# Kernel tuning notes

Hardware: AMD Instinct MI355X
Metric: run time of the kernel (lower is better)

Reference implementation:

```python
import jax, jax.numpy as jnp
import numpy as np

INF = 1.0e6
SIGMA = 1.0
RADIUS = 2.5
M, N, H, K, C_IN, C_OUT = 50000, 50000, 32, 15, 128, 128
EXTENT = 10.0  # spatial extent of the random point cloud


def setup_inputs() -> dict:
    key = jax.random.key(0)
    k1, k2, k3, k4, k5, k6 = jax.random.split(key, 6)
    q_pts = jax.random.uniform(k1, (M, 3), dtype=jnp.float32) * EXTENT
    s_pts = jax.random.uniform(k2, (N, 3), dtype=jnp.float32) * EXTENT
    s_feats = jax.random.normal(k3, (N, C_IN), dtype=jnp.float32)
    neighb_inds = jax.random.randint(k4, (M, H), 0, N, dtype=jnp.int64)
    # kernel points: random points inside sphere of given radius (stand-in for load_kernels)
    kp = jax.random.normal(k5, (K, 3), dtype=jnp.float32)
    kp = kp / jnp.linalg.norm(kp, axis=1, keepdims=True) * (RADIUS * 0.66)
    kernel_points = kp.at[0].set(0.0)  # fixed center point
    # kaiming-uniform-like init
    bound = 1.0 / np.sqrt(C_IN)
    weights = jax.random.uniform(k6, (K, C_IN, C_OUT), dtype=jnp.float32,
                                 minval=-bound, maxval=bound)
    return {"q_pts": q_pts, "s_pts": s_pts, "s_feats": s_feats,
            "neighb_inds": neighb_inds, "kernel_points": kernel_points,
            "weights": weights}


def reference(q_pts, s_pts, s_feats, neighb_inds, kernel_points, weights):
    # pad support points with a far-away point so out-of-range indices get zero influence
    s_pts_pad = jnp.concatenate([s_pts, jnp.full((1, 3), INF, s_pts.dtype)], axis=0)
    neighbors = s_pts_pad[neighb_inds] - q_pts[:, None, :]          # (M, H, 3)
    diffs = neighbors[:, :, None, :] - kernel_points[None, None]    # (M, H, K, 3)
    sq_dist = jnp.sum(diffs * diffs, axis=-1)                       # (M, H, K)
    # linear influence, clipped at 0 (no_grad in torch -> stop_gradient here)
    w = jnp.clip(1.0 - jnp.sqrt(sq_dist) / SIGMA, 0.0)              # (M, H, K)
    neighbor_weights = jax.lax.stop_gradient(jnp.swapaxes(w, 1, 2)) # (M, K, H)
    # gather neighbor features (padded with a zero row)
    feats_pad = jnp.concatenate([s_feats, jnp.zeros((1, s_feats.shape[1]), s_feats.dtype)], axis=0)
    neighbor_feats = feats_pad[neighb_inds]                         # (M, H, C_in)
    weighted_feats = jnp.matmul(neighbor_weights, neighbor_feats)   # (M, K, C_in)
    return jnp.einsum('mkc,kcd->md', weighted_feats, weights)       # (M, C_out)
```

## Files before the change

### kernel.cpp

```cpp
#include <hip/hip_runtime.h>

#define M_Q 50000
#define N_S 50000
#define H_N 32
#define K_P 15
#define C_IN 128
#define C_OUT 128

#define G_QB 64
#define G_NT 256
#define NB_GEO ((M_Q + G_QB - 1) / G_QB)
#define LCAP 64
#define ACC_STRIDE 132

#define WTF_SLOTS (K_P * 8 * 4 * 64)
#define NB_WCVT (WTF_SLOTS / 256)
#define WS_NEED (WTF_SLOTS * 16)

typedef __attribute__((ext_vector_type(8))) short s8v;
typedef __attribute__((ext_vector_type(4))) float f4v;
typedef __attribute__((ext_vector_type(4))) float fl4;
typedef __attribute__((ext_vector_type(4))) unsigned u4v;

static __device__ __forceinline__ unsigned f2bf_bits(float x) {
    union { float f; unsigned u; } v; v.f = x;
    return (v.u + 0x7fffu + ((v.u >> 16) & 1u)) >> 16;
}
static __device__ __forceinline__ unsigned pack_bf16(float a, float b) {
    return f2bf_bits(a) | (f2bf_bits(b) << 16);
}

static __device__ __forceinline__ void lds_fadd(float* p, float v) {
    unsigned off = (unsigned)(unsigned long long)p;
    asm volatile("ds_add_f32 %0, %1" :: "v"(off), "v"(v));
}

__global__ __launch_bounds__(256) void k0_wcvt(
    const float* __restrict__ W, unsigned short* __restrict__ wtf)
{
    const int i = blockIdx.x * 256 + threadIdx.x;
    if (i >= WTF_SLOTS) return;
    const int lane = i & 63;
    const int kk = (i >> 6) & 3;
    const int col = (i >> 8) & 7;
    const int k = i >> 11;
    const int d = col * 16 + (lane & 15);
    const int c0 = kk * 32 + (lane >> 4) * 8;
    u4v g;
    unsigned short* gs = (unsigned short*)&g;
    #pragma unroll
    for (int j = 0; j < 8; ++j)
        gs[j] = (unsigned short)f2bf_bits(W[((size_t)k * 128 + c0 + j) * 128 + d]);
    *(u4v*)(wtf + (size_t)i * 8) = g;
}

template <typename IT>
__global__ __launch_bounds__(G_NT, 3) void kpconv_fused(
    const float* __restrict__ q_pts,
    const float* __restrict__ s_pts,
    const float* __restrict__ s_feats,
    const IT* __restrict__ inds,
    const float* __restrict__ kp,
    const unsigned short* __restrict__ wtf,
    float* __restrict__ out)
{
    __shared__ float s_kp[K_P * 3];
    __shared__ float s_q[G_QB * 3];
    __shared__ int s_lcnt[K_P];
    __shared__ uint2 s_le[K_P][LCAP];
    __shared__ float s_acc[G_QB][ACC_STRIDE];

    const int b = blockIdx.x;
    const int t = threadIdx.x;
    const int qbase = b * G_QB;

    if (t < K_P * 3) s_kp[t] = kp[t];
    if (t < K_P) s_lcnt[t] = 0;
    if (t < G_QB * 3) {
        const int g = qbase * 3 + t;
        s_q[t] = (g < M_Q * 3) ? q_pts[g] : 0.0f;
    }
    {
        fl4* a4 = (fl4*)&s_acc[0][0];
        const fl4 z = {0.0f, 0.0f, 0.0f, 0.0f};
        #pragma unroll
        for (int i = t; i < G_QB * ACC_STRIDE / 4; i += G_NT) a4[i] = z;
    }
    __syncthreads();

    #pragma unroll
    for (int it = 0; it < 8; ++it) {
        const int task = it * G_NT + t;
        const int q = task >> 5, h = task & 31;
        const int qg = qbase + q;
        if (qg < M_Q) {
            long long idx = (long long)inds[(size_t)qg * H_N + h];
            if ((unsigned long long)idx < (unsigned long long)N_S) {
                const int i32 = (int)idx;
                const float rx = s_pts[i32 * 3 + 0] - s_q[q * 3 + 0];
                const float ry = s_pts[i32 * 3 + 1] - s_q[q * 3 + 1];
                const float rz = s_pts[i32 * 3 + 2] - s_q[q * 3 + 2];
                #pragma unroll
                for (int k = 0; k < K_P; ++k) {
                    const float dx = rx - s_kp[k * 3 + 0];
                    const float dy = ry - s_kp[k * 3 + 1];
                    const float dz = rz - s_kp[k * 3 + 2];
                    const float d2 = dx * dx + dy * dy + dz * dz;
                    if (d2 < 1.0f) {
                        const float wgt = 1.0f - sqrtf(d2);
                        const int pos = atomicAdd(&s_lcnt[k], 1);
                        if (pos < LCAP)
                            s_le[k][pos] = make_uint2(((unsigned)q << 16) | (unsigned)i32,
                                                      __float_as_uint(wgt));
                    }
                }
            }
        }
    }
    __syncthreads();

    const int lane = t & 63;
    const int w = t >> 6;
    const int quad = lane >> 4, l15 = lane & 15;

    for (int k = w; k < K_P; k += 4) {
        const int cnt = min(s_lcnt[k], LCAP);
        const unsigned short* wk = wtf + (size_t)k * 2048 * 8;
        for (int sub = 0; sub * 16 < cnt; ++sub) {
            const int e = sub * 16 + l15;
            uint2 ent = make_uint2(0u, 0u);
            if (e < cnt) ent = s_le[k][e];
            const float wgt = __uint_as_float(ent.y);
            const float* fr = s_feats + (size_t)(ent.x & 0xffffu) * C_IN + quad * 8;
            s8v af[4];
            #pragma unroll
            for (int kk = 0; kk < 4; ++kk) {
                const fl4 a  = *(const fl4*)(fr + kk * 32);
                const fl4 bb = *(const fl4*)(fr + kk * 32 + 4);
                u4v g;
                g[0] = pack_bf16(wgt * a.x,  wgt * a.y);
                g[1] = pack_bf16(wgt * a.z,  wgt * a.w);
                g[2] = pack_bf16(wgt * bb.x, wgt * bb.y);
                g[3] = pack_bf16(wgt * bb.z, wgt * bb.w);
                af[kk] = *(s8v*)&g;
            }
            int m4[4];
            #pragma unroll
            for (int r = 0; r < 4; ++r) {
                const int er = sub * 16 + quad * 4 + r;
                m4[r] = (er < cnt) ? (int)(s_le[k][er].x >> 16) : -1;
            }
            #pragma unroll
            for (int nc = 0; nc < 8; ++nc) {
                s8v bfr[4];
                #pragma unroll
                for (int kk = 0; kk < 4; ++kk)
                    bfr[kk] = *(const s8v*)(wk + (size_t)((nc * 4 + kk) * 64 + lane) * 8);
                f4v acc = {0.0f, 0.0f, 0.0f, 0.0f};
                #pragma unroll
                for (int kk = 0; kk < 4; ++kk)
                    acc = __builtin_amdgcn_mfma_f32_16x16x32_bf16(af[kk], bfr[kk], acc, 0, 0, 0);
                #pragma unroll
                for (int r = 0; r < 4; ++r)
                    if (m4[r] >= 0)
                        lds_fadd(&s_acc[m4[r]][nc * 16 + l15], acc[r]);
            }
        }
    }
    asm volatile("s_waitcnt lgkmcnt(0)" ::: "memory");
    __syncthreads();

    const int mmax = min(G_QB, M_Q - qbase);
    #pragma unroll
    for (int it = 0; it < 8; ++it) {
        const int idx = it * G_NT + t;
        const int row = idx >> 5, c4 = (idx & 31) * 4;
        if (row < mmax)
            *(fl4*)(out + (size_t)(qbase + row) * C_OUT + c4) = *(const fl4*)&s_acc[row][c4];
    }
}

template <typename IT>
__global__ __launch_bounds__(128, 8) void kpconv_v1(
    const float* __restrict__ q_pts, const float* __restrict__ s_pts,
    const float* __restrict__ s_feats, const IT* __restrict__ neighb_inds,
    const float* __restrict__ kernel_points, const float* __restrict__ weights,
    float* __restrict__ out)
{
    __shared__ float s_kp[K_P * 3];
    __shared__ float s_w[K_P][H_N];
    __shared__ int s_idx[H_N];
    __shared__ unsigned s_hmask, s_kmask;
    __shared__ float s_wf[K_P][C_IN];
    const int m = blockIdx.x, tid = threadIdx.x;
    if (tid < K_P * 3) s_kp[tid] = kernel_points[tid];
    if (tid == 0) { s_hmask = 0u; s_kmask = 0u; }
    __syncthreads();
    if (tid < H_N) {
        long long idx = (long long)neighb_inds[(size_t)m * H_N + tid];
        const float qx = q_pts[m * 3], qy = q_pts[m * 3 + 1], qz = q_pts[m * 3 + 2];
        float rx, ry, rz; int idx32;
        if ((unsigned long long)idx < (unsigned long long)N_S) {
            idx32 = (int)idx;
            rx = s_pts[idx32 * 3] - qx; ry = s_pts[idx32 * 3 + 1] - qy; rz = s_pts[idx32 * 3 + 2] - qz;
        } else { idx32 = 0; rx = ry = rz = 1.0e6f; }
        s_idx[tid] = idx32;
        unsigned kmask = 0u;
        #pragma unroll
        for (int k = 0; k < K_P; ++k) {
            const float dx = rx - s_kp[k * 3], dy = ry - s_kp[k * 3 + 1], dz = rz - s_kp[k * 3 + 2];
            const float w = fmaxf(1.0f - sqrtf(dx * dx + dy * dy + dz * dz), 0.0f);
            s_w[k][tid] = w;
            if (w > 0.0f) kmask |= (1u << k);
        }
        if (kmask) { atomicOr(&s_hmask, 1u << tid); atomicOr(&s_kmask, kmask); }
    }
    __syncthreads();
    const unsigned hmask = s_hmask, kmask = s_kmask;
    float wf[K_P];
    #pragma unroll
    for (int k = 0; k < K_P; ++k) wf[k] = 0.0f;
    unsigned hmv = hmask;
    while (hmv) {
        const int h = __builtin_ctz(hmv); hmv &= hmv - 1;
        const float f = s_feats[(size_t)s_idx[h] * C_IN + tid];
        #pragma unroll
        for (int k = 0; k < K_P; ++k) wf[k] = fmaf(s_w[k][h], f, wf[k]);
    }
    #pragma unroll
    for (int k = 0; k < K_P; ++k) s_wf[k][tid] = wf[k];
    __syncthreads();
    float a = 0.0f;
    unsigned km = kmask;
    while (km) {
        const int k = __builtin_ctz(km); km &= km - 1;
        const float* Wk = weights + (size_t)k * C_IN * C_OUT + tid;
        #pragma unroll 8
        for (int c = 0; c < C_IN; ++c) a = fmaf(s_wf[k][c], Wk[(size_t)c * C_OUT], a);
    }
    out[(size_t)m * C_OUT + tid] = a;
}

extern "C" void kernel_launch(void* const* d_in, const int* in_sizes, int n_in,
                              void* d_out, int out_size, void* d_ws, size_t ws_size,
                              hipStream_t stream) {
    const float* q_pts         = (const float*)d_in[0];
    const float* s_pts         = (const float*)d_in[1];
    const float* s_feats       = (const float*)d_in[2];
    const float* kernel_points = (const float*)d_in[4];
    const float* weights       = (const float*)d_in[5];
    float* out = (float*)d_out;
    const bool i64 = (in_sizes[3] == 2 * M_Q * H_N);

    if (ws_size < (size_t)WS_NEED) {
        dim3 grid(M_Q), block(128);
        if (i64)
            kpconv_v1<long long><<<grid, block, 0, stream>>>(
                q_pts, s_pts, s_feats, (const long long*)d_in[3], kernel_points, weights, out);
        else
            kpconv_v1<int><<<grid, block, 0, stream>>>(
                q_pts, s_pts, s_feats, (const int*)d_in[3], kernel_points, weights, out);
        return;
    }

    unsigned short* wtf = (unsigned short*)d_ws;
    k0_wcvt<<<dim3(NB_WCVT), dim3(256), 0, stream>>>(weights, wtf);

    dim3 g(NB_GEO), bl(G_NT);
    if (i64)
        kpconv_fused<long long><<<g, bl, 0, stream>>>(
            q_pts, s_pts, s_feats, (const long long*)d_in[3], kernel_points, wtf, out);
    else
        kpconv_fused<int><<<g, bl, 0, stream>>>(
            q_pts, s_pts, s_feats, (const int*)d_in[3], kernel_points, wtf, out);
}
```

Measured before the change: 194.0 us.

## Split fused kernel into geometry bucketing and GEMM kernels, merge weight conversion

Splits the fused kernel into two. The first kernel computes neighbor-to-kernel-point buckets per query block and writes them, with their counts, to workspace; the same launch also holds the bf16 weight conversion as extra blocks. The second kernel loads the buckets and runs the MFMA accumulation with the large LDS accumulator. This separates the geometry phase, which needs little LDS, from the GEMM phase, which needs a lot, so each can reach better occupancy. The cost is a workspace round trip and one more launch boundary.

After: 184.1 us. 1.05x faster.

```diff
diff --git a/kernel.cpp b/kernel.cpp
--- a/kernel.cpp
+++ b/kernel.cpp
@@ -15,7 +15,13 @@
 
 #define WTF_SLOTS (K_P * 8 * 4 * 64)
 #define NB_WCVT (WTF_SLOTS / 256)
-#define WS_NEED (WTF_SLOTS * 16)
+
+#define WS_CNT_OFF 0
+#define WS_WTF_OFF 47104
+#define WS_WTF_BYTES (WTF_SLOTS * 16)
+#define WS_BKT_OFF (WS_WTF_OFF + WS_WTF_BYTES)
+#define WS_BKT_BYTES (NB_GEO * K_P * LCAP * 8)
+#define WS_NEED (WS_BKT_OFF + WS_BKT_BYTES)
 
 typedef __attribute__((ext_vector_type(8))) short s8v;
 typedef __attribute__((ext_vector_type(4))) float f4v;
@@ -35,56 +41,50 @@
     asm volatile("ds_add_f32 %0, %1" :: "v"(off), "v"(v));
 }
 
-__global__ __launch_bounds__(256) void k0_wcvt(
-    const float* __restrict__ W, unsigned short* __restrict__ wtf)
-{
-    const int i = blockIdx.x * 256 + threadIdx.x;
-    if (i >= WTF_SLOTS) return;
-    const int lane = i & 63;
-    const int kk = (i >> 6) & 3;
-    const int col = (i >> 8) & 7;
-    const int k = i >> 11;
-    const int d = col * 16 + (lane & 15);
-    const int c0 = kk * 32 + (lane >> 4) * 8;
-    u4v g;
-    unsigned short* gs = (unsigned short*)&g;
-    #pragma unroll
-    for (int j = 0; j < 8; ++j)
-        gs[j] = (unsigned short)f2bf_bits(W[((size_t)k * 128 + c0 + j) * 128 + d]);
-    *(u4v*)(wtf + (size_t)i * 8) = g;
-}
-
 template <typename IT>
-__global__ __launch_bounds__(G_NT, 3) void kpconv_fused(
+__global__ __launch_bounds__(G_NT) void k1_geom(
     const float* __restrict__ q_pts,
     const float* __restrict__ s_pts,
-    const float* __restrict__ s_feats,
     const IT* __restrict__ inds,
     const float* __restrict__ kp,
-    const unsigned short* __restrict__ wtf,
-    float* __restrict__ out)
+    const float* __restrict__ W,
+    unsigned* __restrict__ ws_u)
 {
+    const int b = blockIdx.x;
+    const int t = threadIdx.x;
+
+    if (b >= NB_GEO) {
+        const int i = (b - NB_GEO) * 256 + t;
+        if (i < WTF_SLOTS) {
+            const int lane = i & 63;
+            const int kk = (i >> 6) & 3;
+            const int col = (i >> 8) & 7;
+            const int k = i >> 11;
+            const int d = col * 16 + (lane & 15);
+            const int c0 = kk * 32 + (lane >> 4) * 8;
+            unsigned short* dst =
+                (unsigned short*)((char*)ws_u + WS_WTF_OFF) + (size_t)i * 8;
+            u4v g;
+            unsigned short* gs = (unsigned short*)&g;
+            #pragma unroll
+            for (int j = 0; j < 8; ++j)
+                gs[j] = (unsigned short)f2bf_bits(W[((size_t)k * 128 + c0 + j) * 128 + d]);
+            *(u4v*)dst = g;
+        }
+        return;
+    }
+
     __shared__ float s_kp[K_P * 3];
     __shared__ float s_q[G_QB * 3];
     __shared__ int s_lcnt[K_P];
     __shared__ uint2 s_le[K_P][LCAP];
-    __shared__ float s_acc[G_QB][ACC_STRIDE];
-
-    const int b = blockIdx.x;
-    const int t = threadIdx.x;
+
     const int qbase = b * G_QB;
-
     if (t < K_P * 3) s_kp[t] = kp[t];
     if (t < K_P) s_lcnt[t] = 0;
     if (t < G_QB * 3) {
         const int g = qbase * 3 + t;
         s_q[t] = (g < M_Q * 3) ? q_pts[g] : 0.0f;
-    }
-    {
-        fl4* a4 = (fl4*)&s_acc[0][0];
-        const fl4 z = {0.0f, 0.0f, 0.0f, 0.0f};
-        #pragma unroll
-        for (int i = t; i < G_QB * ACC_STRIDE / 4; i += G_NT) a4[i] = z;
     }
     __syncthreads();
 
@@ -119,12 +119,53 @@
     }
     __syncthreads();
 
+    uint2* bkt = (uint2*)((char*)ws_u + WS_BKT_OFF) + (size_t)b * (K_P * LCAP);
+    #pragma unroll
+    for (int k = 0; k < K_P; ++k) {
+        if (t < min(s_lcnt[k], LCAP))
+            bkt[k * LCAP + t] = s_le[k][t];
+    }
+    if (t < K_P)
+        ((int*)ws_u)[b * K_P + t] = min(s_lcnt[t], LCAP);
+}
+
+__global__ __launch_bounds__(G_NT, 3) void k2_gemm(
+    const float* __restrict__ s_feats,
+    const unsigned* __restrict__ ws_u,
+    float* __restrict__ out)
+{
+    __shared__ float s_acc[G_QB][ACC_STRIDE];
+    __shared__ uint2 s_le[K_P][LCAP];
+    __shared__ int s_cnt[K_P];
+
+    const int b = blockIdx.x;
+    const int t = threadIdx.x;
+    const int qbase = b * G_QB;
+
+    {
+        fl4* a4 = (fl4*)&s_acc[0][0];
+        const fl4 z = {0.0f, 0.0f, 0.0f, 0.0f};
+        #pragma unroll
+        for (int i = t; i < G_QB * ACC_STRIDE / 4; i += G_NT) a4[i] = z;
+    }
+    {
+        const uint2* bkt = (const uint2*)((const char*)ws_u + WS_BKT_OFF)
+                           + (size_t)b * (K_P * LCAP);
+        uint2* sl = &s_le[0][0];
+        #pragma unroll
+        for (int i = t; i < K_P * LCAP; i += G_NT) sl[i] = bkt[i];
+    }
+    if (t < K_P) s_cnt[t] = ((const int*)ws_u)[b * K_P + t];
+    __syncthreads();
+
+    const unsigned short* wtf = (const unsigned short*)((const char*)ws_u + WS_WTF_OFF);
+
     const int lane = t & 63;
     const int w = t >> 6;
     const int quad = lane >> 4, l15 = lane & 15;
 
     for (int k = w; k < K_P; k += 4) {
-        const int cnt = min(s_lcnt[k], LCAP);
+        const int cnt = min(s_cnt[k], LCAP);
         const unsigned short* wk = wtf + (size_t)k * 2048 * 8;
         for (int sub = 0; sub * 16 < cnt; ++sub) {
             const int e = sub * 16 + l15;
@@ -263,14 +304,16 @@
         return;
     }
 
-    unsigned short* wtf = (unsigned short*)d_ws;
-    k0_wcvt<<<dim3(NB_WCVT), dim3(256), 0, stream>>>(weights, wtf);
-
-    dim3 g(NB_GEO), bl(G_NT);
+    unsigned* ws_u = (unsigned*)d_ws;
+
+    dim3 g1(NB_GEO + NB_WCVT), b1(G_NT);
     if (i64)
-        kpconv_fused<long long><<<g, bl, 0, stream>>>(
-            q_pts, s_pts, s_feats, (const long long*)d_in[3], kernel_points, wtf, out);
+        k1_geom<long long><<<g1, b1, 0, stream>>>(
+            q_pts, s_pts, (const long long*)d_in[3], kernel_points, weights, ws_u);
     else
-        kpconv_fused<int><<<g, bl, 0, stream>>>(
-            q_pts, s_pts, s_feats, (const int*)d_in[3], kernel_points, wtf, out);
-}
+        k1_geom<int><<<g1, b1, 0, stream>>>(
+            q_pts, s_pts, (const int*)d_in[3], kernel_points, weights, ws_u);
+
+    dim3 g2(NB_GEO), b2(G_NT);
+    k2_gemm<<<g2, b2, 0, stream>>>(s_feats, ws_u, out);
+}
```
